# Optimization experiments

Measured on AMD Instinct MI355X. Metric: run time of the kernel, lower is better.

Reference implementation:

```python
import jax, jax.numpy as jnp
import numpy as np

RADIUS = 5
KS = 2 * RADIUS + 1  # 11
SIGMA_X2 = 4.0 ** 2  # 16
SIGMA_I2 = 10.0 ** 2  # 100


def _patches(x):
    """x: [N,1,H,W] -> [N, H*W, KS, KS] zero-padded sliding windows (torch Unfold semantics)."""
    N, _, H, W = x.shape
    p = jax.lax.conv_general_dilated_patches(
        x, (KS, KS), (1, 1), [(RADIUS, RADIUS), (RADIUS, RADIUS)]
    )  # [N, KS*KS, H, W], channel dim ordered (kh, kw)
    return p.reshape(N, KS, KS, H * W).transpose(0, 3, 1, 2)


def _distance_map(dtype):
    d = (jnp.arange(KS, dtype=dtype) - RADIUS) ** 2
    return jnp.exp(-(d[:, None] + d[None, :]) / SIGMA_X2)  # [KS, KS]


def setup_inputs() -> dict:
    key = jax.random.key(0)
    k1, k2 = jax.random.split(key)
    images = jax.random.uniform(k1, (8, 1, 224, 224), dtype=jnp.float32)
    labels = jax.random.uniform(k2, (8, 4, 224, 224), dtype=jnp.float32)
    return {"images": images, "labels": labels}


def reference(images, labels):
    B, _, H, W = images.shape
    K = labels.shape[1]
    HW = H * W

    img = images * 255.0
    regions = _patches(img)                                   # [B,HW,KS,KS]
    mask = _patches(jnp.ones((1, 1, H, W), img.dtype))        # [1,HW,KS,KS], 0 on padding
    dist_map = _distance_map(img.dtype)                       # [KS,KS]

    i_f = img.reshape(B, HW)[:, :, None, None]                # center pixel intensity
    weights = dist_map * jnp.exp(-(regions - i_f) ** 2 / SIGMA_I2) * mask  # [B,HW,KS,KS]

    # class-prob patches for all classes at once
    P = _patches(labels.reshape(B * K, 1, H, W)).reshape(B, K, HW, KS, KS)

    num = jnp.einsum('bnij,bknij->bkn', weights, P)           # sum_j w_ij * p_j
    den = weights.sum(axis=(2, 3))                            # [B,HW], sum_j w_ij
    p_f = labels.reshape(B, K, HW)

    ratio = jnp.einsum('bkn,bkn->bk', p_f, num) / jnp.einsum('bkn,bn->bk', p_f, den)
    # per-class L1Loss(ratio, 0) = mean over batch of |ratio|; summed over classes
    ratio_sum = jnp.abs(ratio).mean(axis=0).sum()
    return K - ratio_sum
```

## Files before the change

kernel.cpp:

```cpp
#include <hip/hip_runtime.h>
#include <hip/hip_bf16.h>

constexpr int Hh = 224;
constexpr int Ww = 224;
constexpr int Bb = 8;
constexpr int Kc = 4;
constexpr int RAD = 5;
constexpr int KS = 11;

constexpr int TX = 32;
constexpr int TY = 8;
constexpr int SW = TX + 2 * RAD;
constexpr int SH = TY + 2 * RAD;
constexpr int SSTR = SW + 1;

__global__ __launch_bounds__(256) void ncut_main(const float* __restrict__ images,
                                                 const float* __restrict__ labels,
                                                 float* __restrict__ acc ) {
    __shared__ float  simg[SH * SSTR];
    __shared__ float4 slab[SH * SSTR];

    const int b   = blockIdx.z;
    const int x0  = blockIdx.x * TX;
    const int y0  = blockIdx.y * TY;
    const int tid = threadIdx.x;

    const float* imgb = images + (size_t)b * (Hh * Ww);
    const float* labb = labels + (size_t)b * (Kc * Hh * Ww);

    for (int idx = tid; idx < SH * SW; idx += 256) {
        const int lx = idx % SW, ly = idx / SW;
        const int gx = x0 - RAD + lx, gy = y0 - RAD + ly;
        float  iv = 1e19f;
        float4 lv = make_float4(0.f, 0.f, 0.f, 0.f);
        if (gx >= 0 && gx < Ww && gy >= 0 && gy < Hh) {
            const int g = gy * Ww + gx;
            iv = imgb[g] * 255.0f;
            lv.x = labb[g];
            lv.y = labb[Hh * Ww + g];
            lv.z = labb[2 * Hh * Ww + g];
            lv.w = labb[3 * Hh * Ww + g];
        }
        simg[ly * SSTR + lx] = iv;
        slab[ly * SSTR + lx] = lv;
    }
    __syncthreads();

    const int tx = tid & (TX - 1);
    const int ty = tid >> 5;

    const float c = simg[(ty + RAD) * SSTR + (tx + RAD)];

    float  den = 0.f;
    float4 num = make_float4(0.f, 0.f, 0.f, 0.f);

    constexpr float d2[KS] = {25.f, 16.f, 9.f, 4.f, 1.f, 0.f, 1.f, 4.f, 9.f, 16.f, 25.f};

    for (int dy = 0; dy < KS; ++dy) {
        const float ndy = -d2[dy] * 0.0625f;
        const int rowbase = (ty + dy) * SSTR + tx;
#pragma unroll
        for (int dx = 0; dx < KS; ++dx) {
            const float v    = simg[rowbase + dx];
            const float diff = v - c;
            const float e = __expf(fmaf(diff * diff, -0.01f, ndy - d2[dx] * 0.0625f));
            const float4 p = slab[rowbase + dx];
            den   += e;
            num.x  = fmaf(e, p.x, num.x);
            num.y  = fmaf(e, p.y, num.y);
            num.z  = fmaf(e, p.z, num.z);
            num.w  = fmaf(e, p.w, num.w);
        }
    }

    const float4 pc = slab[(ty + RAD) * SSTR + (tx + RAD)];

    float vals[8] = {pc.x * num.x, pc.y * num.y, pc.z * num.z, pc.w * num.w,
                     pc.x * den,   pc.y * den,   pc.z * den,   pc.w * den};

#pragma unroll
    for (int i = 0; i < 8; ++i) {
        float v = vals[i];
#pragma unroll
        for (int off = 32; off > 0; off >>= 1) v += __shfl_down(v, off, 64);
        vals[i] = v;
    }

    __shared__ float red[4][8];
    const int wave = tid >> 6;
    const int lane = tid & 63;
    if (lane == 0) {
#pragma unroll
        for (int i = 0; i < 8; ++i) red[wave][i] = vals[i];
    }
    __syncthreads();

    if (tid < 8) {
        const float s = red[0][tid] + red[1][tid] + red[2][tid] + red[3][tid];
        const int k     = tid & 3;
        const int isden = tid >> 2;
        atomicAdd(&acc[isden * 32 + b * Kc + k], s);
    }
}

__global__ void ncut_final(const float* __restrict__ acc, float* __restrict__ out) {
    const int tid = threadIdx.x;
    float r = 0.f;
    if (tid < 32) {
        r = fabsf(acc[tid] / acc[32 + tid]);
    }
#pragma unroll
    for (int off = 32; off > 0; off >>= 1) r += __shfl_down(r, off, 64);
    if (tid == 0) out[0] = (float)Kc - r * (1.0f / (float)Bb);
}

extern "C" void kernel_launch(void* const* d_in, const int* in_sizes, int n_in,
                              void* d_out, int out_size, void* d_ws, size_t ws_size,
                              hipStream_t stream) {
    const float* images = (const float*)d_in[0];
    const float* labels = (const float*)d_in[1];
    float* out = (float*)d_out;
    float* acc = (float*)d_ws;

    hipMemsetAsync(acc, 0, 64 * sizeof(float), stream);

    dim3 grid(Ww / TX, Hh / TY, Bb);
    ncut_main<<<grid, 256, 0, stream>>>(images, labels, acc);
    ncut_final<<<1, 64, 0, stream>>>(acc, out);
}
```

Before: 90.66 us.

## Compute two output rows per thread, use exp2, and replace atomics with partial sums

Each thread now computes two vertically adjacent output pixels. This lets it share the shared-memory loads of image and label values across both 11x11 windows and halves the number of tiles in the y direction. The exponential is rewritten as exp2 with constants prescaled by log2(e), using packed float2 arithmetic. Global atomics and the memset are replaced by per-block partial sums written to workspace, which the final kernel then reduces serially. The cost is more register pressure from the extra accumulators, a longer serial loop in the final kernel, and half as many blocks in the grid.

```diff
diff --git a/kernel.cpp b/kernel.cpp
--- a/kernel.cpp
+++ b/kernel.cpp
@@ -1,82 +1,109 @@
 #include <hip/hip_runtime.h>
 #include <hip/hip_bf16.h>
 
-constexpr int Hh = 224;
-constexpr int Ww = 224;
-constexpr int Bb = 8;
-constexpr int Kc = 4;
-constexpr int RAD = 5;
-constexpr int KS = 11;
+typedef float f2 __attribute__((ext_vector_type(2)));
+typedef float f4 __attribute__((ext_vector_type(4)));
+
+constexpr int Hh = 224, Ww = 224, Bb = 8, Kc = 4, RAD = 5;
 
 constexpr int TX = 32;
-constexpr int TY = 8;
+constexpr int TILEH = 16;
 constexpr int SW = TX + 2 * RAD;
-constexpr int SH = TY + 2 * RAD;
+constexpr int SH = TILEH + 2 * RAD;
 constexpr int SSTR = SW + 1;
+constexpr int GXD = Ww / TX;
+constexpr int GYD = Hh / TILEH;
+constexpr int PB = GXD * GYD;
 
-__global__ __launch_bounds__(256) void ncut_main(const float* __restrict__ images,
-                                                 const float* __restrict__ labels,
-                                                 float* __restrict__ acc ) {
-    __shared__ float  simg[SH * SSTR];
-    __shared__ float4 slab[SH * SSTR];
+constexpr float LOG2E = 1.44269504f;
+constexpr float KI = -0.01f * LOG2E;
+constexpr float DSC = -0.0625f * LOG2E;
+constexpr float D2[12] = {25.f,16.f,9.f,4.f,1.f,0.f,1.f,4.f,9.f,16.f,25.f,0.f};
+
+static __device__ inline f4 splat4(float x) { return (f4){x, x, x, x}; }
+
+__global__ __launch_bounds__(256, 3) void ncut_main(const float* __restrict__ images,
+                                                    const float* __restrict__ labels,
+                                                    float* __restrict__ acc) {
+    __shared__ float simg[SH * SSTR];
+    __shared__ f4    slab[SH * SSTR];
+    __shared__ float red[4][8];
 
     const int b   = blockIdx.z;
     const int x0  = blockIdx.x * TX;
-    const int y0  = blockIdx.y * TY;
+    const int y0  = blockIdx.y * TILEH;
     const int tid = threadIdx.x;
 
     const float* imgb = images + (size_t)b * (Hh * Ww);
     const float* labb = labels + (size_t)b * (Kc * Hh * Ww);
 
-    for (int idx = tid; idx < SH * SW; idx += 256) {
-        const int lx = idx % SW, ly = idx / SW;
+    for (int idx = tid; idx < SH * SSTR; idx += 256) {
+        const int lx = idx % SSTR, ly = idx / SSTR;
         const int gx = x0 - RAD + lx, gy = y0 - RAD + ly;
-        float  iv = 1e19f;
-        float4 lv = make_float4(0.f, 0.f, 0.f, 0.f);
-        if (gx >= 0 && gx < Ww && gy >= 0 && gy < Hh) {
+        float iv = 1e19f;
+        f4 lv = (f4){0.f, 0.f, 0.f, 0.f};
+        if (lx < SW && gx >= 0 && gx < Ww && gy >= 0 && gy < Hh) {
             const int g = gy * Ww + gx;
             iv = imgb[g] * 255.0f;
-            lv.x = labb[g];
-            lv.y = labb[Hh * Ww + g];
-            lv.z = labb[2 * Hh * Ww + g];
-            lv.w = labb[3 * Hh * Ww + g];
+            lv = (f4){labb[g], labb[Hh * Ww + g], labb[2 * Hh * Ww + g], labb[3 * Hh * Ww + g]};
         }
-        simg[ly * SSTR + lx] = iv;
-        slab[ly * SSTR + lx] = lv;
+        simg[idx] = iv;
+        slab[idx] = lv;
     }
     __syncthreads();
 
-    const int tx = tid & (TX - 1);
+    const int tx = tid & 31;
     const int ty = tid >> 5;
+    const int r0 = 2 * ty;
 
-    const float c = simg[(ty + RAD) * SSTR + (tx + RAD)];
+    const float c0 = simg[(r0 + RAD) * SSTR + tx + RAD];
+    const float c1 = simg[(r0 + RAD + 1) * SSTR + tx + RAD];
 
-    float  den = 0.f;
-    float4 num = make_float4(0.f, 0.f, 0.f, 0.f);
+    f4 num0 = splat4(0.f), num1 = splat4(0.f);
+    f2 den0 = (f2){0.f, 0.f}, den1 = (f2){0.f, 0.f};
 
-    constexpr float d2[KS] = {25.f, 16.f, 9.f, 4.f, 1.f, 0.f, 1.f, 4.f, 9.f, 16.f, 25.f};
-
-    for (int dy = 0; dy < KS; ++dy) {
-        const float ndy = -d2[dy] * 0.0625f;
-        const int rowbase = (ty + dy) * SSTR + tx;
 #pragma unroll
-        for (int dx = 0; dx < KS; ++dx) {
-            const float v    = simg[rowbase + dx];
-            const float diff = v - c;
-            const float e = __expf(fmaf(diff * diff, -0.01f, ndy - d2[dx] * 0.0625f));
-            const float4 p = slab[rowbase + dx];
-            den   += e;
-            num.x  = fmaf(e, p.x, num.x);
-            num.y  = fmaf(e, p.y, num.y);
-            num.z  = fmaf(e, p.z, num.z);
-            num.w  = fmaf(e, p.w, num.w);
+    for (int dr = 0; dr < 12; ++dr) {
+        const int rowoff = (r0 + dr) * SSTR + tx;
+#pragma unroll
+        for (int i = 0; i < 6; ++i) {
+            const f2 v  = (f2){simg[rowoff + 2 * i], simg[rowoff + 2 * i + 1]};
+            const f4 p0 = slab[rowoff + 2 * i];
+            const f4 p1 = slab[rowoff + 2 * i + 1];
+            if (dr < 11) {
+                const f2 base = (f2){(D2[2 * i] + D2[dr]) * DSC,
+                                     (D2[2 * i + 1] + D2[dr]) * DSC};
+                const f2 d = v - c0;
+                const f2 a = __builtin_elementwise_fma(d * KI, d, base);
+                const float e0 = __builtin_amdgcn_exp2f(a.x);
+                const float e1 = __builtin_amdgcn_exp2f(a.y);
+                den0 += (f2){e0, e1};
+                num0 = __builtin_elementwise_fma(splat4(e0), p0, num0);
+                num0 = __builtin_elementwise_fma(splat4(e1), p1, num0);
+            }
+            if (dr >= 1) {
+                const f2 base = (f2){(D2[2 * i] + D2[dr - 1]) * DSC,
+                                     (D2[2 * i + 1] + D2[dr - 1]) * DSC};
+                const f2 d = v - c1;
+                const f2 a = __builtin_elementwise_fma(d * KI, d, base);
+                const float e0 = __builtin_amdgcn_exp2f(a.x);
+                const float e1 = __builtin_amdgcn_exp2f(a.y);
+                den1 += (f2){e0, e1};
+                num1 = __builtin_elementwise_fma(splat4(e0), p0, num1);
+                num1 = __builtin_elementwise_fma(splat4(e1), p1, num1);
+            }
         }
     }
 
-    const float4 pc = slab[(ty + RAD) * SSTR + (tx + RAD)];
+    const f4 pc0 = slab[(r0 + RAD) * SSTR + tx + RAD];
+    const f4 pc1 = slab[(r0 + RAD + 1) * SSTR + tx + RAD];
+    const float dn0 = den0.x + den0.y;
+    const float dn1 = den1.x + den1.y;
 
-    float vals[8] = {pc.x * num.x, pc.y * num.y, pc.z * num.z, pc.w * num.w,
-                     pc.x * den,   pc.y * den,   pc.z * den,   pc.w * den};
+    const f4 numv = pc0 * num0 + pc1 * num1;
+    const f4 denv = pc0 * dn0 + pc1 * dn1;
+
+    float vals[8] = {numv.x, numv.y, numv.z, numv.w, denv.x, denv.y, denv.z, denv.w};
 
 #pragma unroll
     for (int i = 0; i < 8; ++i) {
@@ -86,9 +113,7 @@
         vals[i] = v;
     }
 
-    __shared__ float red[4][8];
-    const int wave = tid >> 6;
-    const int lane = tid & 63;
+    const int wave = tid >> 6, lane = tid & 63;
     if (lane == 0) {
 #pragma unroll
         for (int i = 0; i < 8; ++i) red[wave][i] = vals[i];
@@ -96,22 +121,21 @@
     __syncthreads();
 
     if (tid < 8) {
-        const float s = red[0][tid] + red[1][tid] + red[2][tid] + red[3][tid];
-        const int k     = tid & 3;
-        const int isden = tid >> 2;
-        atomicAdd(&acc[isden * 32 + b * Kc + k], s);
+        const int gid = blockIdx.x + GXD * blockIdx.y + GXD * GYD * blockIdx.z;
+        acc[gid * 8 + tid] = red[0][tid] + red[1][tid] + red[2][tid] + red[3][tid];
     }
 }
 
 __global__ void ncut_final(const float* __restrict__ acc, float* __restrict__ out) {
-    const int tid = threadIdx.x;
-    float r = 0.f;
-    if (tid < 32) {
-        r = fabsf(acc[tid] / acc[32 + tid]);
-    }
+    const int t = threadIdx.x;
+    const int k = t & 3, b = (t >> 2) & 7, part = t >> 5;
+    float s = 0.f;
+    for (int j = 0; j < PB; ++j) s += acc[(b * PB + j) * 8 + k + 4 * part];
+    const float den = __shfl(s, (t + 32) & 63, 64);
+    float r = (t < 32) ? fabsf(s / den) : 0.f;
 #pragma unroll
     for (int off = 32; off > 0; off >>= 1) r += __shfl_down(r, off, 64);
-    if (tid == 0) out[0] = (float)Kc - r * (1.0f / (float)Bb);
+    if (t == 0) out[0] = (float)Kc - r * (1.0f / (float)Bb);
 }
 
 extern "C" void kernel_launch(void* const* d_in, const int* in_sizes, int n_in,
@@ -122,9 +146,7 @@
     float* out = (float*)d_out;
     float* acc = (float*)d_ws;
 
-    hipMemsetAsync(acc, 0, 64 * sizeof(float), stream);
-
-    dim3 grid(Ww / TX, Hh / TY, Bb);
+    dim3 grid(GXD, GYD, Bb);
     ncut_main<<<grid, 256, 0, stream>>>(images, labels, acc);
     ncut_final<<<1, 64, 0, stream>>>(acc, out);
 }
```

New measurement: 83.95 us. 7.4% less time.
